# Performance work log

Measured on AMD Instinct MI355X. Metric: run time of the kernel, lower is better.

## Reference

```python
import jax, jax.numpy as jnp
import numpy as np

Q = 8192      # num query tokens
S = 32768     # num support points
E = 131072    # num edges (query<-support neighbor pairs)
D = 256       # token_dim
H = 8         # num_heads
HD = D // H   # head_dim = 32
GEO = 128     # geo mlp_hidden = geo_dim
FFN = 2 * D   # ffn hidden
STAT_IN = 12  # 4 stats * 3 coords
EPS_LN = 1e-5


def gelu(x):
    return jax.nn.gelu(x, approximate=False)  # torch nn.GELU default (erf)


def layernorm(x, g, b):
    m = jnp.mean(x, axis=-1, keepdims=True)
    v = jnp.mean((x - m) ** 2, axis=-1, keepdims=True)
    return (x - m) * jax.lax.rsqrt(v + EPS_LN) * g + b


def setup_inputs() -> dict:
    key = jax.random.key(0)
    ks = jax.random.split(key, 16)
    w = lambda k, shp: jax.random.normal(k, shp, jnp.float32) * 0.02
    return {
        "query_tokens": jax.random.normal(ks[0], (Q, D), jnp.float32),
        "query_pos": jax.random.normal(ks[1], (Q, 3), jnp.float32),
        "support_feats": jax.random.normal(ks[2], (S, D), jnp.float32),
        "support_pos": jax.random.normal(ks[3], (S, 3), jnp.float32),
        "Wq": w(ks[4], (D, D)), "Wk": w(ks[5], (D, D)), "Wv": w(ks[6], (D, D)),
        "Wg": w(ks[7], (GEO, D)),
        "Wo": w(ks[8], (D, D)), "bo": jnp.zeros((D,), jnp.float32),
        "log_tau": jnp.array(0.0, jnp.float32),
        "ln1_g": jnp.ones((D,), jnp.float32), "ln1_b": jnp.zeros((D,), jnp.float32),
        "ln2_g": jnp.ones((D,), jnp.float32), "ln2_b": jnp.zeros((D,), jnp.float32),
        "Wf1": w(ks[9], (D, FFN)), "bf1": jnp.zeros((FFN,), jnp.float32),
        "Wf2": w(ks[10], (FFN, D)), "bf2": jnp.zeros((D,), jnp.float32),
        "Gw1": w(ks[11], (STAT_IN, GEO)), "Gb1": jnp.zeros((GEO,), jnp.float32),
        "Gw2": w(ks[12], (GEO, GEO)), "Gb2": jnp.zeros((GEO,), jnp.float32),
        "q_idx": jnp.sort(jax.random.randint(ks[13], (E,), 0, Q)),
        "s_idx": jax.random.randint(ks[14], (E,), 0, S),
        "num_queries": Q,
    }


def geo_stats(rel, q_idx, num_q):
    # rel: [E,3] relative positions; segmented mean/std/min/max -> [num_q, 12]
    ones = jnp.ones((rel.shape[0], 1), rel.dtype)
    cnt = jnp.maximum(jax.ops.segment_sum(ones, q_idx, num_q), 1.0)  # [Q,1]
    mean = jax.ops.segment_sum(rel, q_idx, num_q) / cnt
    var = jax.ops.segment_sum((rel - mean[q_idx]) ** 2, q_idx, num_q) / cnt
    std = jnp.sqrt(var)
    # torch inits min/max with +/-inf then clamps to [-100,100]; jax segment
    # min/max init with dtype extremes -> same result after clip
    mn = jnp.clip(jax.ops.segment_min(rel, q_idx, num_q), -100.0, 100.0)
    mx = jnp.clip(jax.ops.segment_max(rel, q_idx, num_q), -100.0, 100.0)
    return jnp.concatenate([mean, std, mn, mx], axis=-1)


def reference(query_tokens, query_pos, support_feats, support_pos,
              Wq, Wk, Wv, Wg, Wo, bo, log_tau,
              ln1_g, ln1_b, ln2_g, ln2_b,
              Wf1, bf1, Wf2, bf2, Gw1, Gb1, Gw2, Gb2,
              q_idx, s_idx, num_queries):
    num_q = num_queries
    # ---- statistical geo embedding ----
    rel = support_pos[s_idx] - query_pos[q_idx]                 # [E,3]
    raw = geo_stats(rel, q_idx, num_q)                          # [Q,12]
    geo = gelu(gelu(raw @ Gw1 + Gb1) @ Gw2 + Gb2)               # [Q,GEO]

    # ---- AGNO cross attention (pre-norm) ----
    qt = layernorm(query_tokens, ln1_g, ln1_b)
    Qf = qt @ Wq                                                # [Q,D]
    Kf = support_feats @ Wk                                     # [S,D]
    Vf = support_feats @ Wv                                     # [S,D]
    Gf = geo @ Wg                                               # [Q,D]
    qh = Qf[q_idx].reshape(E, H, HD)
    kh = Kf[s_idx].reshape(E, H, HD)
    vh = Vf[s_idx].reshape(E, H, HD)
    gh = Gf[q_idx].reshape(E, H, HD)
    tau = jnp.exp(log_tau)
    scores = jnp.sum(qh * kh, axis=-1) / (jnp.sqrt(jnp.float32(HD)) * tau)  # [E,H]
    # torch scores_max starts at 0 -> max(0, segment max)
    smax = jnp.maximum(jax.ops.segment_max(scores, q_idx, num_q), 0.0)
    ex = jnp.exp(scores - smax[q_idx])
    ssum = jax.ops.segment_sum(ex, q_idx, num_q)
    alpha = ex / jnp.maximum(ssum[q_idx], 1e-8)                 # [E,H]
    weighted = alpha[..., None] * (vh + gh)                     # [E,H,HD]
    out = jax.ops.segment_sum(weighted, q_idx, num_q)           # [Q,H,HD]
    attn = out.reshape(num_q, D) @ Wo + bo

    # ---- residual + FFN ----
    x = query_tokens + attn
    x = x + gelu(layernorm(x, ln2_g, ln2_b) @ Wf1 + bf1) @ Wf2 + bf2
    return x
```

## Files before the change

kernel.cpp:

```cpp
#include <hip/hip_runtime.h>
#include <math.h>

#define QN 8192
#define SN 32768
#define EN 131072
#define DN 256
#define HN 8
#define HDN 32
#define GEON 128
#define FFNN 512

typedef __attribute__((ext_vector_type(8))) short bf16x8;
typedef __attribute__((ext_vector_type(8))) unsigned short u16x8;
typedef __attribute__((ext_vector_type(4))) unsigned short u16x4;
typedef __attribute__((ext_vector_type(4))) float f32x4;

__device__ __forceinline__ unsigned short f2b(float f) {
  union { float f; unsigned u; } v; v.f = f;
  unsigned u = v.u;
  u += 0x7fffu + ((u >> 16) & 1u);
  return (unsigned short)(u >> 16);
}
__device__ __forceinline__ float b2f(unsigned short h) {
  union { unsigned u; float f; } v; v.u = ((unsigned)h) << 16; return v.f;
}
__device__ __forceinline__ float gelu_f(float x) {
  return 0.5f * x * (1.0f + erff(x * 0.70710678118654752440f));
}

__device__ __forceinline__ void tr_one(long idx, const float* src, unsigned short* dst, int K, int N) {
  int n = (int)(idx / K);
  int k = (int)(idx % K);
  dst[idx] = f2b(src[(size_t)k * N + n]);
}

__global__ __launch_bounds__(256) void prep_weights(
    const float* Wq, const float* Wk, const float* Wv, const float* Wg,
    const float* Wo, const float* Wf1, const float* Wf2,
    unsigned short* WqT, unsigned short* WkvT, unsigned short* WgT,
    unsigned short* WoT, unsigned short* Wf1T, unsigned short* Wf2T) {
  long i = (long)blockIdx.x * 256 + threadIdx.x;
  if (i < 65536)        tr_one(i,          Wq,  WqT,          256, 256);
  else if (i < 131072)  tr_one(i - 65536,  Wk,  WkvT,         256, 256);
  else if (i < 196608)  tr_one(i - 131072, Wv,  WkvT + 65536, 256, 256);
  else if (i < 229376)  tr_one(i - 196608, Wg,  WgT,          128, 256);
  else if (i < 294912)  tr_one(i - 229376, Wo,  WoT,          256, 256);
  else if (i < 425984)  tr_one(i - 294912, Wf1, Wf1T,         256, 512);
  else if (i < 557056)  tr_one(i - 425984, Wf2, Wf2T,         512, 256);
}

__global__ __launch_bounds__(256) void seg_offsets(const int* q_idx, int* offs) {
  int i = blockIdx.x * 256 + threadIdx.x;
  if (i > QN) return;
  int lo = 0, hi = EN;
  while (lo < hi) {
    int mid = (lo + hi) >> 1;
    if (q_idx[mid] < i) lo = mid + 1; else hi = mid;
  }
  offs[i] = lo;
}

__global__ __launch_bounds__(256) void geo_stats_kernel(
    const float* qpos, const float* spos, const int* offs, const int* s_idx, float* raw) {
  int q = blockIdx.x * 64 + (threadIdx.x >> 2);
  int sub = threadIdx.x & 3;
  int e0 = offs[q], e1 = offs[q + 1];
  float qx = qpos[q * 3 + 0], qy = qpos[q * 3 + 1], qz = qpos[q * 3 + 2];
  float cnt = 0.f, sx = 0.f, sy = 0.f, sz = 0.f, sxx = 0.f, syy = 0.f, szz = 0.f;
  float mnx = 1e30f, mny = 1e30f, mnz = 1e30f, mxx = -1e30f, mxy = -1e30f, mxz = -1e30f;
  for (int e = e0 + sub; e < e1; e += 4) {
    int s = s_idx[e];
    float rx = spos[s * 3 + 0] - qx;
    float ry = spos[s * 3 + 1] - qy;
    float rz = spos[s * 3 + 2] - qz;
    cnt += 1.f;
    sx += rx; sy += ry; sz += rz;
    sxx += rx * rx; syy += ry * ry; szz += rz * rz;
    mnx = fminf(mnx, rx); mny = fminf(mny, ry); mnz = fminf(mnz, rz);
    mxx = fmaxf(mxx, rx); mxy = fmaxf(mxy, ry); mxz = fmaxf(mxz, rz);
  }
#pragma unroll
  for (int msk = 1; msk <= 2; msk <<= 1) {
    cnt += __shfl_xor(cnt, msk);
    sx += __shfl_xor(sx, msk); sy += __shfl_xor(sy, msk); sz += __shfl_xor(sz, msk);
    sxx += __shfl_xor(sxx, msk); syy += __shfl_xor(syy, msk); szz += __shfl_xor(szz, msk);
    mnx = fminf(mnx, __shfl_xor(mnx, msk));
    mny = fminf(mny, __shfl_xor(mny, msk));
    mnz = fminf(mnz, __shfl_xor(mnz, msk));
    mxx = fmaxf(mxx, __shfl_xor(mxx, msk));
    mxy = fmaxf(mxy, __shfl_xor(mxy, msk));
    mxz = fmaxf(mxz, __shfl_xor(mxz, msk));
  }
  if (sub == 0) {
    float c = fmaxf(cnt, 1.f);
    float mx_ = sx / c, my_ = sy / c, mz_ = sz / c;
    float vx = fmaxf(sxx / c - mx_ * mx_, 0.f);
    float vy = fmaxf(syy / c - my_ * my_, 0.f);
    float vz = fmaxf(szz / c - mz_ * mz_, 0.f);
    float* r = raw + (size_t)q * 12;
    r[0] = mx_; r[1] = my_; r[2] = mz_;
    r[3] = sqrtf(vx); r[4] = sqrtf(vy); r[5] = sqrtf(vz);
    r[6] = fminf(fmaxf(mnx, -100.f), 100.f);
    r[7] = fminf(fmaxf(mny, -100.f), 100.f);
    r[8] = fminf(fmaxf(mnz, -100.f), 100.f);
    r[9] = fminf(fmaxf(mxx, -100.f), 100.f);
    r[10] = fminf(fmaxf(mxy, -100.f), 100.f);
    r[11] = fminf(fmaxf(mxz, -100.f), 100.f);
  }
}

__global__ __launch_bounds__(128) void geo_mlp_kernel(
    const float* raw, const float* Gw1, const float* Gb1,
    const float* Gw2, const float* Gb2, unsigned short* geo_b) {
  int qb = blockIdx.x * 8;
  int j = threadIdx.x;
  __shared__ float rs[8][12];
  __shared__ float h1[8][128];
  if (j < 96) rs[j / 12][j % 12] = raw[(size_t)(qb + j / 12) * 12 + (j % 12)];
  __syncthreads();
  float b1 = Gb1[j];
  float acc[8];
#pragma unroll
  for (int qq = 0; qq < 8; ++qq) acc[qq] = b1;
  for (int i = 0; i < 12; ++i) {
    float w = Gw1[i * GEON + j];
#pragma unroll
    for (int qq = 0; qq < 8; ++qq) acc[qq] += rs[qq][i] * w;
  }
#pragma unroll
  for (int qq = 0; qq < 8; ++qq) h1[qq][j] = gelu_f(acc[qq]);
  __syncthreads();
  float b2 = Gb2[j];
  float acc2[8];
#pragma unroll
  for (int qq = 0; qq < 8; ++qq) acc2[qq] = b2;
  for (int k = 0; k < 128; ++k) {
    float w = Gw2[k * GEON + j];
#pragma unroll
    for (int qq = 0; qq < 8; ++qq) acc2[qq] += h1[qq][k] * w;
  }
#pragma unroll
  for (int qq = 0; qq < 8; ++qq)
    geo_b[(size_t)(qb + qq) * GEON + j] = f2b(gelu_f(acc2[qq]));
}

__global__ __launch_bounds__(256) void ln_kernel(
    const float* x, const float* g, const float* b, unsigned short* out) {
  int row = blockIdx.x * 4 + (threadIdx.x >> 6);
  int lane = threadIdx.x & 63;
  const float* xr = x + (size_t)row * DN;
  float4 v = *(const float4*)(xr + lane * 4);
  float s = v.x + v.y + v.z + v.w;
  float ss = v.x * v.x + v.y * v.y + v.z * v.z + v.w * v.w;
#pragma unroll
  for (int msk = 1; msk <= 32; msk <<= 1) {
    s += __shfl_xor(s, msk);
    ss += __shfl_xor(ss, msk);
  }
  float mean = s * (1.f / 256.f);
  float var = ss * (1.f / 256.f) - mean * mean;
  float rs = 1.0f / sqrtf(var + 1e-5f);
  float4 gg = *(const float4*)(g + lane * 4);
  float4 bb = *(const float4*)(b + lane * 4);
  unsigned short* o = out + (size_t)row * DN + lane * 4;
  o[0] = f2b((v.x - mean) * rs * gg.x + bb.x);
  o[1] = f2b((v.y - mean) * rs * gg.y + bb.y);
  o[2] = f2b((v.z - mean) * rs * gg.z + bb.z);
  o[3] = f2b((v.w - mean) * rs * gg.w + bb.w);
}

template <bool A_FP32, bool COLGRID, bool HAS_BIAS, bool DO_GELU, bool HAS_RESID, bool STORE_F32>
__global__ __launch_bounds__(256) void gemm64(
    const void* Ap, const unsigned short* BT, int M, int N, int K,
    const float* bias, const float* resid, float* outF, unsigned short* outB) {
  __shared__ unsigned short As[64][40];
  __shared__ unsigned short Bs[64][40];
  int t = threadIdx.x;
  int bm = (COLGRID ? blockIdx.x : blockIdx.y) * 64;
  int bn = (COLGRID ? blockIdx.y : blockIdx.x) * 64;
  int w = t >> 6, lane = t & 63;
  int wr = w >> 1, wc = w & 1;
  int quad = lane >> 4, l16 = lane & 15;
  int row = t >> 2, chunk = t & 3;

  f32x4 acc[2][2];
#pragma unroll
  for (int i = 0; i < 2; ++i)
#pragma unroll
    for (int j = 0; j < 2; ++j) acc[i][j] = (f32x4){0.f, 0.f, 0.f, 0.f};

  for (int k0 = 0; k0 < K; k0 += 32) {
    if (A_FP32) {
      const float* Ag = (const float*)Ap + (size_t)(bm + row) * K + k0 + chunk * 8;
      float4 f0 = *(const float4*)Ag;
      float4 f1 = *(const float4*)(Ag + 4);
      u16x8 u;
      u[0] = f2b(f0.x); u[1] = f2b(f0.y); u[2] = f2b(f0.z); u[3] = f2b(f0.w);
      u[4] = f2b(f1.x); u[5] = f2b(f1.y); u[6] = f2b(f1.z); u[7] = f2b(f1.w);
      *reinterpret_cast<u16x8*>(&As[row][chunk * 8]) = u;
    } else {
      const unsigned short* Ag = (const unsigned short*)Ap + (size_t)(bm + row) * K + k0 + chunk * 8;
      *reinterpret_cast<u16x8*>(&As[row][chunk * 8]) = *reinterpret_cast<const u16x8*>(Ag);
    }
    {
      const unsigned short* Bg = BT + (size_t)(bn + row) * K + k0 + chunk * 8;
      *reinterpret_cast<u16x8*>(&Bs[row][chunk * 8]) = *reinterpret_cast<const u16x8*>(Bg);
    }
    __syncthreads();
    bf16x8 a0 = *reinterpret_cast<const bf16x8*>(&As[wr * 32 + l16][quad * 8]);
    bf16x8 a1 = *reinterpret_cast<const bf16x8*>(&As[wr * 32 + 16 + l16][quad * 8]);
    bf16x8 b0 = *reinterpret_cast<const bf16x8*>(&Bs[wc * 32 + l16][quad * 8]);
    bf16x8 b1 = *reinterpret_cast<const bf16x8*>(&Bs[wc * 32 + 16 + l16][quad * 8]);
    acc[0][0] = __builtin_amdgcn_mfma_f32_16x16x32_bf16(a0, b0, acc[0][0], 0, 0, 0);
    acc[0][1] = __builtin_amdgcn_mfma_f32_16x16x32_bf16(a0, b1, acc[0][1], 0, 0, 0);
    acc[1][0] = __builtin_amdgcn_mfma_f32_16x16x32_bf16(a1, b0, acc[1][0], 0, 0, 0);
    acc[1][1] = __builtin_amdgcn_mfma_f32_16x16x32_bf16(a1, b1, acc[1][1], 0, 0, 0);
    __syncthreads();
  }

#pragma unroll
  for (int i = 0; i < 2; ++i)
#pragma unroll
    for (int j = 0; j < 2; ++j) {
      int col = bn + wc * 32 + j * 16 + l16;
      float bv = HAS_BIAS ? bias[col] : 0.f;
#pragma unroll
      for (int r = 0; r < 4; ++r) {
        int rw = bm + wr * 32 + i * 16 + quad * 4 + r;
        float v = acc[i][j][r] + bv;
        if (DO_GELU) v = gelu_f(v);
        if (HAS_RESID) v += resid[(size_t)rw * N + col];
        if (STORE_F32) outF[(size_t)rw * N + col] = v;
        else outB[(size_t)rw * N + col] = f2b(v);
      }
    }
}

__global__ __launch_bounds__(256) void attn_edge_kernel(
    const unsigned short* Qb, const float* Gf, const unsigned short* KVb,
    const int* s_idx, const int* offs, const float* log_tau, unsigned short* attn_b) {
  int q = blockIdx.x * 4 + (threadIdx.x >> 6);
  int lane = threadIdx.x & 63;
  int e0 = offs[q], e1 = offs[q + 1];
  float invs = expf(-log_tau[0]) * 0.17677669529663687f;
  int d0 = lane * 4;
  u16x4 qu = *(const u16x4*)(Qb + (size_t)q * DN + d0);
  float q0 = b2f(qu[0]) * invs, q1 = b2f(qu[1]) * invs, q2 = b2f(qu[2]) * invs, q3 = b2f(qu[3]) * invs;
  float4 gv = *(const float4*)(Gf + (size_t)q * DN + d0);
  float m = -INFINITY, l = 0.f;
  float a0 = 0.f, a1 = 0.f, a2 = 0.f, a3 = 0.f;
  for (int e = e0; e < e1; ++e) {
    int s = s_idx[e];
    const unsigned short* kr = KVb + (size_t)s * 512 + d0;
    u16x4 ku = *(const u16x4*)kr;
    u16x4 vu = *(const u16x4*)(kr + 256);
    float p = q0 * b2f(ku[0]) + q1 * b2f(ku[1]) + q2 * b2f(ku[2]) + q3 * b2f(ku[3]);
    p += __shfl_xor(p, 1);
    p += __shfl_xor(p, 2);
    p += __shfl_xor(p, 4);
    float mnew = fmaxf(m, p);
    float sc = expf(m - mnew);
    float we = expf(p - mnew);
    l = l * sc + we;
    a0 = a0 * sc + we * (b2f(vu[0]) + gv.x);
    a1 = a1 * sc + we * (b2f(vu[1]) + gv.y);
    a2 = a2 * sc + we * (b2f(vu[2]) + gv.z);
    a3 = a3 * sc + we * (b2f(vu[3]) + gv.w);
    m = mnew;
  }
  float M = fmaxf(m, 0.f);
  float em = expf(m - M);
  float denom = fmaxf(l * em, 1e-8f);
  float f = em / denom;
  unsigned short* o = attn_b + (size_t)q * DN + d0;
  o[0] = f2b(a0 * f); o[1] = f2b(a1 * f); o[2] = f2b(a2 * f); o[3] = f2b(a3 * f);
}

extern "C" void kernel_launch(void* const* d_in, const int* in_sizes, int n_in,
                              void* d_out, int out_size, void* d_ws, size_t ws_size,
                              hipStream_t stream) {
  const float* query_tokens  = (const float*)d_in[0];
  const float* query_pos     = (const float*)d_in[1];
  const float* support_feats = (const float*)d_in[2];
  const float* support_pos   = (const float*)d_in[3];
  const float* Wq  = (const float*)d_in[4];
  const float* Wk  = (const float*)d_in[5];
  const float* Wv  = (const float*)d_in[6];
  const float* Wg  = (const float*)d_in[7];
  const float* Wo  = (const float*)d_in[8];
  const float* bo  = (const float*)d_in[9];
  const float* log_tau = (const float*)d_in[10];
  const float* ln1_g = (const float*)d_in[11];
  const float* ln1_b = (const float*)d_in[12];
  const float* ln2_g = (const float*)d_in[13];
  const float* ln2_b = (const float*)d_in[14];
  const float* Wf1 = (const float*)d_in[15];
  const float* bf1 = (const float*)d_in[16];
  const float* Wf2 = (const float*)d_in[17];
  const float* bf2 = (const float*)d_in[18];
  const float* Gw1 = (const float*)d_in[19];
  const float* Gb1 = (const float*)d_in[20];
  const float* Gw2 = (const float*)d_in[21];
  const float* Gb2 = (const float*)d_in[22];
  const int* q_idx = (const int*)d_in[23];
  const int* s_idx = (const int*)d_in[24];
  float* out = (float*)d_out;

  char* ws = (char*)d_ws;
  size_t off = 0;
  auto alloc = [&](size_t bytes) -> void* {
    void* p = ws + off;
    off = (off + bytes + 255) & ~(size_t)255;
    return p;
  };
  unsigned short* WqT  = (unsigned short*)alloc(65536 * 2);
  unsigned short* WkvT = (unsigned short*)alloc(131072 * 2);
  unsigned short* WgT  = (unsigned short*)alloc(32768 * 2);
  unsigned short* WoT  = (unsigned short*)alloc(65536 * 2);
  unsigned short* Wf1T = (unsigned short*)alloc(131072 * 2);
  unsigned short* Wf2T = (unsigned short*)alloc(131072 * 2);
  int* offs            = (int*)alloc((QN + 1) * 4);
  float* raw           = (float*)alloc((size_t)QN * 12 * 4);
  unsigned short* geo_b = (unsigned short*)alloc((size_t)QN * GEON * 2);
  unsigned short* qt_b  = (unsigned short*)alloc((size_t)QN * DN * 2);
  unsigned short* Qb    = (unsigned short*)alloc((size_t)QN * DN * 2);
  float* GfBuf          = (float*)alloc((size_t)QN * DN * 4);
  unsigned short* KVb   = (unsigned short*)alloc((size_t)SN * 512 * 2);
  unsigned short* attn_b = (unsigned short*)alloc((size_t)QN * DN * 2);
  float* x1             = (float*)alloc((size_t)QN * DN * 4);
  unsigned short* z_b   = (unsigned short*)alloc((size_t)QN * DN * 2);
  unsigned short* h_b   = (unsigned short*)alloc((size_t)QN * FFNN * 2);

  prep_weights<<<2176, 256, 0, stream>>>(Wq, Wk, Wv, Wg, Wo, Wf1, Wf2,
                                         WqT, WkvT, WgT, WoT, Wf1T, Wf2T);
  seg_offsets<<<33, 256, 0, stream>>>(q_idx, offs);
  geo_stats_kernel<<<QN / 64, 256, 0, stream>>>(query_pos, support_pos, offs, s_idx, raw);
  geo_mlp_kernel<<<QN / 8, 128, 0, stream>>>(raw, Gw1, Gb1, Gw2, Gb2, geo_b);
  ln_kernel<<<QN / 4, 256, 0, stream>>>(query_tokens, ln1_g, ln1_b, qt_b);
  gemm64<true, true, false, false, false, false><<<dim3(SN / 64, 512 / 64), 256, 0, stream>>>(
      support_feats, WkvT, SN, 512, 256, nullptr, nullptr, nullptr, KVb);
  gemm64<false, true, false, false, false, false><<<dim3(QN / 64, DN / 64), 256, 0, stream>>>(
      qt_b, WqT, QN, DN, 256, nullptr, nullptr, nullptr, Qb);
  gemm64<false, true, false, false, false, true><<<dim3(QN / 64, DN / 64), 256, 0, stream>>>(
      geo_b, WgT, QN, DN, 128, nullptr, nullptr, GfBuf, nullptr);
  attn_edge_kernel<<<QN / 4, 256, 0, stream>>>(Qb, GfBuf, KVb, s_idx, offs, log_tau, attn_b);
  gemm64<false, true, true, false, true, true><<<dim3(QN / 64, DN / 64), 256, 0, stream>>>(
      attn_b, WoT, QN, DN, 256, bo, query_tokens, x1, nullptr);
  ln_kernel<<<QN / 4, 256, 0, stream>>>(x1, ln2_g, ln2_b, z_b);
  gemm64<false, true, true, true, false, false><<<dim3(QN / 64, FFNN / 64), 256, 0, stream>>>(
      z_b, Wf1T, QN, FFNN, 256, bf1, nullptr, nullptr, h_b);
  gemm64<false, true, true, false, true, true><<<dim3(QN / 64, DN / 64), 256, 0, stream>>>(
      h_b, Wf2T, QN, DN, 512, bf2, x1, out, nullptr);

  (void)in_sizes; (void)n_in; (void)out_size; (void)ws_size;
}
```

Measured before the change: 258.7 us.

## Tile weight transpose, add resident-A KV GEMM, split edges across half-waves, bf16 Gf

Replaces the scalar weight transpose with a 64x64 shared-memory tiled transpose that uses vector loads and stores. Adds a dedicated KV GEMM that converts each 64-row block of support features to bf16 once, keeps it in swizzled LDS, and loops over all output column tiles, so the fp32 input is no longer reread once per column block. The edge attention kernel now gives each half-wave 8 dims per lane and processes two edges at a time, then merges the two online-softmax states by shuffle. Gf is stored in bf16, which halves its traffic at some cost in precision.

```diff
diff --git a/kernel.cpp b/kernel.cpp
--- a/kernel.cpp
+++ b/kernel.cpp
@@ -28,25 +28,42 @@
   return 0.5f * x * (1.0f + erff(x * 0.70710678118654752440f));
 }
 
-__device__ __forceinline__ void tr_one(long idx, const float* src, unsigned short* dst, int K, int N) {
-  int n = (int)(idx / K);
-  int k = (int)(idx % K);
-  dst[idx] = f2b(src[(size_t)k * N + n]);
-}
-
-__global__ __launch_bounds__(256) void prep_weights(
+__global__ __launch_bounds__(256) void transpose_weights(
     const float* Wq, const float* Wk, const float* Wv, const float* Wg,
     const float* Wo, const float* Wf1, const float* Wf2,
     unsigned short* WqT, unsigned short* WkvT, unsigned short* WgT,
     unsigned short* WoT, unsigned short* Wf1T, unsigned short* Wf2T) {
-  long i = (long)blockIdx.x * 256 + threadIdx.x;
-  if (i < 65536)        tr_one(i,          Wq,  WqT,          256, 256);
-  else if (i < 131072)  tr_one(i - 65536,  Wk,  WkvT,         256, 256);
-  else if (i < 196608)  tr_one(i - 131072, Wv,  WkvT + 65536, 256, 256);
-  else if (i < 229376)  tr_one(i - 196608, Wg,  WgT,          128, 256);
-  else if (i < 294912)  tr_one(i - 229376, Wo,  WoT,          256, 256);
-  else if (i < 425984)  tr_one(i - 294912, Wf1, Wf1T,         256, 512);
-  else if (i < 557056)  tr_one(i - 425984, Wf2, Wf2T,         512, 256);
+  int b = blockIdx.x;
+  const float* src; unsigned short* dst; int K, N, tile;
+  if (b < 16)       { src = Wq;  dst = WqT;          K = 256; N = 256; tile = b; }
+  else if (b < 32)  { src = Wk;  dst = WkvT;         K = 256; N = 256; tile = b - 16; }
+  else if (b < 48)  { src = Wv;  dst = WkvT + 65536; K = 256; N = 256; tile = b - 32; }
+  else if (b < 56)  { src = Wg;  dst = WgT;          K = 128; N = 256; tile = b - 48; }
+  else if (b < 72)  { src = Wo;  dst = WoT;          K = 256; N = 256; tile = b - 56; }
+  else if (b < 104) { src = Wf1; dst = Wf1T;         K = 256; N = 512; tile = b - 72; }
+  else              { src = Wf2; dst = Wf2T;         K = 512; N = 256; tile = b - 104; }
+  int ktiles = K >> 6;
+  int k0 = (tile % ktiles) * 64, n0 = (tile / ktiles) * 64;
+  __shared__ float ts[64][65];
+  int t = threadIdx.x;
+  int c4 = (t & 15) * 4;
+  int r = t >> 4;
+#pragma unroll
+  for (int p = 0; p < 4; ++p) {
+    int row = p * 16 + r;
+    float4 v = *(const float4*)(src + (size_t)(k0 + row) * N + n0 + c4);
+    ts[row][c4 + 0] = v.x; ts[row][c4 + 1] = v.y;
+    ts[row][c4 + 2] = v.z; ts[row][c4 + 3] = v.w;
+  }
+  __syncthreads();
+#pragma unroll
+  for (int p = 0; p < 4; ++p) {
+    int n = p * 16 + r;
+    ushort4 o;
+    o.x = f2b(ts[c4 + 0][n]); o.y = f2b(ts[c4 + 1][n]);
+    o.z = f2b(ts[c4 + 2][n]); o.w = f2b(ts[c4 + 3][n]);
+    *(ushort4*)(dst + (size_t)(n0 + n) * K + k0 + c4) = o;
+  }
 }
 
 __global__ __launch_bounds__(256) void seg_offsets(const int* q_idx, int* offs) {
@@ -169,6 +186,64 @@
   o[3] = f2b((v.w - mean) * rs * gg.w + bb.w);
 }
 
+__device__ __forceinline__ u16x8* lds_g(unsigned short* base, int row, int col) {
+  int g = (col >> 3) ^ (row & 7);
+  return reinterpret_cast<u16x8*>(base + row * 256 + g * 8);
+}
+__global__ __launch_bounds__(256) void kv_gemm(
+    const float* A, const unsigned short* BT, unsigned short* KVb) {
+  __shared__ unsigned short As[64 * 256];
+  __shared__ unsigned short Bs[32 * 256];
+  int t = threadIdx.x;
+  int bm = blockIdx.x * 64;
+  int w = t >> 6, lane = t & 63;
+  int quad = lane >> 4, l16 = lane & 15;
+  int wr = w >> 1, wc = w & 1;
+  int srow = t >> 2, sub = t & 3;
+  {
+    const float* Ag = A + (size_t)(bm + srow) * 256 + sub * 64;
+#pragma unroll
+    for (int i = 0; i < 8; ++i) {
+      float4 f0 = *(const float4*)(Ag + i * 8);
+      float4 f1 = *(const float4*)(Ag + i * 8 + 4);
+      u16x8 u;
+      u[0] = f2b(f0.x); u[1] = f2b(f0.y); u[2] = f2b(f0.z); u[3] = f2b(f0.w);
+      u[4] = f2b(f1.x); u[5] = f2b(f1.y); u[6] = f2b(f1.z); u[7] = f2b(f1.w);
+      *lds_g(As, srow, sub * 64 + i * 8) = u;
+    }
+  }
+  int brow = t >> 3, bsub = t & 7;
+  for (int ct = 0; ct < 16; ++ct) {
+    {
+      const unsigned short* Bg = BT + (size_t)(ct * 32 + brow) * 256 + bsub * 32;
+#pragma unroll
+      for (int i = 0; i < 4; ++i)
+        *lds_g(Bs, brow, bsub * 32 + i * 8) = *reinterpret_cast<const u16x8*>(Bg + i * 8);
+    }
+    __syncthreads();
+    f32x4 acc[2];
+    acc[0] = (f32x4){0.f, 0.f, 0.f, 0.f};
+    acc[1] = (f32x4){0.f, 0.f, 0.f, 0.f};
+#pragma unroll
+    for (int k = 0; k < 8; ++k) {
+      bf16x8 a0 = *reinterpret_cast<bf16x8*>(lds_g(As, wr * 32 + l16, k * 32 + quad * 8));
+      bf16x8 a1 = *reinterpret_cast<bf16x8*>(lds_g(As, wr * 32 + 16 + l16, k * 32 + quad * 8));
+      bf16x8 b0 = *reinterpret_cast<bf16x8*>(lds_g(Bs, wc * 16 + l16, k * 32 + quad * 8));
+      acc[0] = __builtin_amdgcn_mfma_f32_16x16x32_bf16(a0, b0, acc[0], 0, 0, 0);
+      acc[1] = __builtin_amdgcn_mfma_f32_16x16x32_bf16(a1, b0, acc[1], 0, 0, 0);
+    }
+#pragma unroll
+    for (int i = 0; i < 2; ++i)
+#pragma unroll
+      for (int r = 0; r < 4; ++r) {
+        int rw = bm + wr * 32 + i * 16 + quad * 4 + r;
+        int col = ct * 32 + wc * 16 + l16;
+        KVb[(size_t)rw * 512 + col] = f2b(acc[i][r]);
+      }
+    __syncthreads();
+  }
+}
+
 template <bool A_FP32, bool COLGRID, bool HAS_BIAS, bool DO_GELU, bool HAS_RESID, bool STORE_F32>
 __global__ __launch_bounds__(256) void gemm64(
     const void* Ap, const unsigned short* BT, int M, int N, int K,
@@ -237,43 +312,67 @@
 }
 
 __global__ __launch_bounds__(256) void attn_edge_kernel(
-    const unsigned short* Qb, const float* Gf, const unsigned short* KVb,
+    const unsigned short* Qb, const unsigned short* Gfb, const unsigned short* KVb,
     const int* s_idx, const int* offs, const float* log_tau, unsigned short* attn_b) {
   int q = blockIdx.x * 4 + (threadIdx.x >> 6);
   int lane = threadIdx.x & 63;
+  int half = lane >> 5;
+  int sl = lane & 31;
+  int d0 = sl * 8;
   int e0 = offs[q], e1 = offs[q + 1];
   float invs = expf(-log_tau[0]) * 0.17677669529663687f;
-  int d0 = lane * 4;
-  u16x4 qu = *(const u16x4*)(Qb + (size_t)q * DN + d0);
-  float q0 = b2f(qu[0]) * invs, q1 = b2f(qu[1]) * invs, q2 = b2f(qu[2]) * invs, q3 = b2f(qu[3]) * invs;
-  float4 gv = *(const float4*)(Gf + (size_t)q * DN + d0);
+  u16x8 qu = *(const u16x8*)(Qb + (size_t)q * DN + d0);
+  u16x8 gu = *(const u16x8*)(Gfb + (size_t)q * DN + d0);
+  float qf[8], gf[8];
+#pragma unroll
+  for (int j = 0; j < 8; ++j) { qf[j] = b2f(qu[j]) * invs; gf[j] = b2f(gu[j]); }
+  const float NEG = -1e30f;
   float m = -INFINITY, l = 0.f;
-  float a0 = 0.f, a1 = 0.f, a2 = 0.f, a3 = 0.f;
-  for (int e = e0; e < e1; ++e) {
-    int s = s_idx[e];
+  float a[8];
+#pragma unroll
+  for (int j = 0; j < 8; ++j) a[j] = 0.f;
+  for (int e = e0; e < e1; e += 2) {
+    int ee = e + half;
+    bool valid = ee < e1;
+    int s = s_idx[valid ? ee : (e1 - 1)];
     const unsigned short* kr = KVb + (size_t)s * 512 + d0;
-    u16x4 ku = *(const u16x4*)kr;
-    u16x4 vu = *(const u16x4*)(kr + 256);
-    float p = q0 * b2f(ku[0]) + q1 * b2f(ku[1]) + q2 * b2f(ku[2]) + q3 * b2f(ku[3]);
+    u16x8 ku = *(const u16x8*)kr;
+    u16x8 vu = *(const u16x8*)(kr + 256);
+    float p = 0.f;
+#pragma unroll
+    for (int j = 0; j < 8; ++j) p += qf[j] * b2f(ku[j]);
     p += __shfl_xor(p, 1);
     p += __shfl_xor(p, 2);
-    p += __shfl_xor(p, 4);
+    if (!valid) p = -INFINITY;
     float mnew = fmaxf(m, p);
-    float sc = expf(m - mnew);
-    float we = expf(p - mnew);
+    float sc = (m > NEG) ? __expf(m - mnew) : 0.f;
+    float we = valid ? __expf(p - mnew) : 0.f;
     l = l * sc + we;
-    a0 = a0 * sc + we * (b2f(vu[0]) + gv.x);
-    a1 = a1 * sc + we * (b2f(vu[1]) + gv.y);
-    a2 = a2 * sc + we * (b2f(vu[2]) + gv.z);
-    a3 = a3 * sc + we * (b2f(vu[3]) + gv.w);
+#pragma unroll
+    for (int j = 0; j < 8; ++j) a[j] = a[j] * sc + we * (b2f(vu[j]) + gf[j]);
     m = mnew;
   }
-  float M = fmaxf(m, 0.f);
-  float em = expf(m - M);
+  float om = __shfl_xor(m, 32);
+  float ol = __shfl_xor(l, 32);
+  float M2 = fmaxf(m, om);
+  float ws = (m > NEG) ? __expf(m - M2) : 0.f;
+  float wo = (om > NEG) ? __expf(om - M2) : 0.f;
+  l = l * ws + ol * wo;
+#pragma unroll
+  for (int j = 0; j < 8; ++j) {
+    float oa = __shfl_xor(a[j], 32);
+    a[j] = a[j] * ws + oa * wo;
+  }
+  float M = fmaxf(M2, 0.f);
+  float em = (M2 > NEG) ? __expf(M2 - M) : 0.f;
   float denom = fmaxf(l * em, 1e-8f);
   float f = em / denom;
-  unsigned short* o = attn_b + (size_t)q * DN + d0;
-  o[0] = f2b(a0 * f); o[1] = f2b(a1 * f); o[2] = f2b(a2 * f); o[3] = f2b(a3 * f);
+  if (half == 0) {
+    u16x8 o;
+#pragma unroll
+    for (int j = 0; j < 8; ++j) o[j] = f2b(a[j] * f);
+    *(u16x8*)(attn_b + (size_t)q * DN + d0) = o;
+  }
 }
 
 extern "C" void kernel_launch(void* const* d_in, const int* in_sizes, int n_in,
@@ -324,26 +423,25 @@
   unsigned short* geo_b = (unsigned short*)alloc((size_t)QN * GEON * 2);
   unsigned short* qt_b  = (unsigned short*)alloc((size_t)QN * DN * 2);
   unsigned short* Qb    = (unsigned short*)alloc((size_t)QN * DN * 2);
-  float* GfBuf          = (float*)alloc((size_t)QN * DN * 4);
+  unsigned short* Gf_b  = (unsigned short*)alloc((size_t)QN * DN * 2);
   unsigned short* KVb   = (unsigned short*)alloc((size_t)SN * 512 * 2);
   unsigned short* attn_b = (unsigned short*)alloc((size_t)QN * DN * 2);
   float* x1             = (float*)alloc((size_t)QN * DN * 4);
   unsigned short* z_b   = (unsigned short*)alloc((size_t)QN * DN * 2);
   unsigned short* h_b   = (unsigned short*)alloc((size_t)QN * FFNN * 2);
 
-  prep_weights<<<2176, 256, 0, stream>>>(Wq, Wk, Wv, Wg, Wo, Wf1, Wf2,
-                                         WqT, WkvT, WgT, WoT, Wf1T, Wf2T);
+  transpose_weights<<<136, 256, 0, stream>>>(Wq, Wk, Wv, Wg, Wo, Wf1, Wf2,
+                                             WqT, WkvT, WgT, WoT, Wf1T, Wf2T);
   seg_offsets<<<33, 256, 0, stream>>>(q_idx, offs);
   geo_stats_kernel<<<QN / 64, 256, 0, stream>>>(query_pos, support_pos, offs, s_idx, raw);
   geo_mlp_kernel<<<QN / 8, 128, 0, stream>>>(raw, Gw1, Gb1, Gw2, Gb2, geo_b);
   ln_kernel<<<QN / 4, 256, 0, stream>>>(query_tokens, ln1_g, ln1_b, qt_b);
-  gemm64<true, true, false, false, false, false><<<dim3(SN / 64, 512 / 64), 256, 0, stream>>>(
-      support_feats, WkvT, SN, 512, 256, nullptr, nullptr, nullptr, KVb);
+  kv_gemm<<<SN / 64, 256, 0, stream>>>(support_feats, WkvT, KVb);
   gemm64<false, true, false, false, false, false><<<dim3(QN / 64, DN / 64), 256, 0, stream>>>(
       qt_b, WqT, QN, DN, 256, nullptr, nullptr, nullptr, Qb);
-  gemm64<false, true, false, false, false, true><<<dim3(QN / 64, DN / 64), 256, 0, stream>>>(
-      geo_b, WgT, QN, DN, 128, nullptr, nullptr, GfBuf, nullptr);
-  attn_edge_kernel<<<QN / 4, 256, 0, stream>>>(Qb, GfBuf, KVb, s_idx, offs, log_tau, attn_b);
+  gemm64<false, true, false, false, false, false><<<dim3(QN / 64, DN / 64), 256, 0, stream>>>(
+      geo_b, WgT, QN, DN, 128, nullptr, nullptr, nullptr, Gf_b);
+  attn_edge_kernel<<<QN / 4, 256, 0, stream>>>(Qb, Gf_b, KVb, s_idx, offs, log_tau, attn_b);
   gemm64<false, true, true, false, true, true><<<dim3(QN / 64, DN / 64), 256, 0, stream>>>(
       attn_b, WoT, QN, DN, 256, bo, query_tokens, x1, nullptr);
   ln_kernel<<<QN / 4, 256, 0, stream>>>(x1, ln2_g, ln2_b, z_b);
```

Result: faster. 250.9 us (-3.0%).
